# Performance work log

Hardware: AMD Instinct MI355X
Metric: run time of the kernel (lower is better)

Reference implementation:

```python
import jax, jax.numpy as jnp
import numpy as np


def setup_inputs() -> dict:
    key = jax.random.key(0)
    k1, k2, k3, k4 = jax.random.split(key, 4)
    B, D_vis, E, N = 512, 4096, 1024, 512
    vf = jax.random.normal(k1, (B, D_vis), dtype=jnp.float32)
    p_lfs = jax.random.normal(k2, (B, E), dtype=jnp.float32)
    n_lfs = jax.random.normal(k3, (N, E), dtype=jnp.float32)
    W = jax.random.normal(k4, (E, D_vis), dtype=jnp.float32) * (1.0 / np.sqrt(D_vis))
    b = jnp.zeros((E,), dtype=jnp.float32)
    return {"vf": vf, "p_lfs": p_lfs, "n_lfs": n_lfs, "W": W, "b": b}


def _partial_order_sim(hypers, hypos):
    # -||relu(hypers - hypos)||_2 along last dim
    act = jax.nn.relu(hypers - hypos)
    return -jnp.sqrt(jnp.sum(act * act, axis=-1))


def reference(vf, p_lfs, n_lfs, W, b):
    # vf: [B, D_vis], W: [E, D_vis] -> vf_emb: [B, E]
    vf_emb = jnp.einsum("bd,ed->be", vf, W) + b
    # positive scores: [B]
    p_scores = _partial_order_sim(p_lfs, vf_emb)
    # negative scores, batched over B: n_lfs [N,E] vs vf_emb [B,E] -> [B,N]
    n_scores = _partial_order_sim(n_lfs[None, :, :], vf_emb[:, None, :])
    # score_stack: [B, 1+N]
    return jnp.concatenate([p_scores[:, None], n_scores], axis=1)
```

## Files before the change

kernel.cpp:

```cpp
#include <hip/hip_runtime.h>
#include <hip/hip_bf16.h>

constexpr int B = 512;
constexpr int D = 4096;
constexpr int E = 1024;
constexpr int N = 512;
constexpr int KS = 4;
constexpr int KC = D / KS;
constexpr int NSTEP = KC / 32;
constexpr int ES = 8;
constexpr int EC = E / ES;

typedef __attribute__((ext_vector_type(8))) short bf16x8;
typedef __attribute__((ext_vector_type(4))) float f32x4;
typedef float v2f __attribute__((ext_vector_type(2)));

typedef __attribute__((address_space(3))) void lds_void;
typedef const __attribute__((address_space(1))) void gbl_void;

__device__ __forceinline__ unsigned short f2bf(float f) {
    __hip_bfloat16 h = __float2bfloat16(f);
    return *reinterpret_cast<unsigned short*>(&h);
}

__global__ __launch_bounds__(256) void cvt_all(
    const float* __restrict__ vf, const float* __restrict__ W,
    unsigned short* __restrict__ vfB, unsigned short* __restrict__ WB)
{
    const int bid = blockIdx.x;
    const float* src;
    unsigned short* dst;
    int i;
    if (bid < 1024) { src = vf; dst = vfB; i = (bid * 256 + threadIdx.x) * 8; }
    else           { src = W;  dst = WB;  i = ((bid - 1024) * 256 + threadIdx.x) * 8; }
    float4 v0 = *(const float4*)(src + i);
    float4 v1 = *(const float4*)(src + i + 4);
    bf16x8 o;
    o[0] = (short)f2bf(v0.x); o[1] = (short)f2bf(v0.y);
    o[2] = (short)f2bf(v0.z); o[3] = (short)f2bf(v0.w);
    o[4] = (short)f2bf(v1.x); o[5] = (short)f2bf(v1.y);
    o[6] = (short)f2bf(v1.z); o[7] = (short)f2bf(v1.w);
    *(bf16x8*)(dst + i) = o;
}

__global__ __launch_bounds__(64) void gemm_lds(
    const unsigned short* __restrict__ vf,
    const unsigned short* __restrict__ W,
    float* __restrict__ part)
{
    __shared__ unsigned short sA[2][2048];
    __shared__ unsigned short sB[2][2048];

    const int L  = threadIdx.x;
    const int n0 = blockIdx.x * 64;
    const int m0 = blockIdx.y * 64;
    const int ks = blockIdx.z;

    const int subrow = L >> 2;
    const int qstg = (L & 3) ^ ((L >> 2) & 3) ^ ((L >> 4) & 3);
    const int kbeg = ks * KC;
    const unsigned short* aSrc[4];
    const unsigned short* bSrc[4];
    #pragma unroll
    for (int c = 0; c < 4; ++c) {
        aSrc[c] = vf + (size_t)(m0 + c * 16 + subrow) * D + kbeg + qstg * 8;
        bSrc[c] = W  + (size_t)(n0 + c * 16 + subrow) * D + kbeg + qstg * 8;
    }

    const int r16 = L & 15;
    const int quad = L >> 4;
    const int swz = quad ^ (r16 & 3) ^ ((r16 >> 2) & 3);
    const int aoff = r16 * 64 + swz * 16;

    f32x4 acc[4][4] = {};

    auto issue = [&](int step, int buf) {
        const size_t koff = (size_t)step * 32;
        #pragma unroll
        for (int c = 0; c < 4; ++c) {
            __builtin_amdgcn_global_load_lds(
                (gbl_void*)(aSrc[c] + koff),
                (lds_void*)((char*)&sA[buf][0] + c * 1024), 16, 0, 0);
            __builtin_amdgcn_global_load_lds(
                (gbl_void*)(bSrc[c] + koff),
                (lds_void*)((char*)&sB[buf][0] + c * 1024), 16, 0, 0);
        }
    };

    issue(0, 0);
    issue(1, 1);

    #pragma unroll 1
    for (int s = 0; s < NSTEP; ++s) {
        const int buf = s & 1;
        if (s == NSTEP - 1) __builtin_amdgcn_s_waitcnt(0x0F70);
        else                __builtin_amdgcn_s_waitcnt(0x0F78);

        bf16x8 af[4], bf_[4];
        #pragma unroll
        for (int i = 0; i < 4; ++i)
            af[i] = *(const bf16x8*)((const char*)&sA[buf][0] + i * 1024 + aoff);
        #pragma unroll
        for (int j = 0; j < 4; ++j)
            bf_[j] = *(const bf16x8*)((const char*)&sB[buf][0] + j * 1024 + aoff);

        #pragma unroll
        for (int i = 0; i < 4; ++i)
            #pragma unroll
            for (int j = 0; j < 4; ++j)
                acc[i][j] = __builtin_amdgcn_mfma_f32_16x16x32_bf16(
                    af[i], bf_[j], acc[i][j], 0, 0, 0);

        if (s + 2 < NSTEP) issue(s + 2, buf);
    }

    float* po = part + (size_t)ks * B * E;
    #pragma unroll
    for (int j = 0; j < 4; ++j) {
        const int col = n0 + j * 16 + r16;
        #pragma unroll
        for (int i = 0; i < 4; ++i) {
            const int row = m0 + i * 16 + quad * 4;
            #pragma unroll
            for (int r = 0; r < 4; ++r)
                po[(size_t)(row + r) * E + col] = acc[i][j][r];
        }
    }
}

__global__ __launch_bounds__(256) void reduce_emb(
    const float* __restrict__ part, const float* __restrict__ bias,
    float* __restrict__ emb)
{
    const int idx = (blockIdx.x * 256 + threadIdx.x) * 4;
    const int col = idx & (E - 1);
    float4 s = *(const float4*)(bias + col);
    #pragma unroll
    for (int ks = 0; ks < KS; ++ks) {
        float4 p = *(const float4*)(part + (size_t)ks * B * E + idx);
        s.x += p.x; s.y += p.y; s.z += p.z; s.w += p.w;
    }
    *(float4*)(emb + idx) = s;
}

__global__ __launch_bounds__(256, 2) void scores_part(
    const float* __restrict__ emb,
    const float* __restrict__ n_lfs,
    float* __restrict__ pn)
{
    constexpr int LDW = EC + 2;
    __shared__ float eS[64 * LDW];
    __shared__ float nS[64 * LDW];

    const int t  = threadIdx.x;
    const int n0 = blockIdx.x * 64;
    const int b0 = blockIdx.y * 64;
    const int e0 = blockIdx.z * EC;

    {
        const int row = t >> 2;
        const int cb  = (t & 3) * 32;
        const float* ep = emb   + (size_t)(b0 + row) * E + e0 + cb;
        const float* np = n_lfs + (size_t)(n0 + row) * E + e0 + cb;
        float* ed = &eS[row * LDW + cb];
        float* nd = &nS[row * LDW + cb];
        #pragma unroll
        for (int q = 0; q < 8; ++q) {
            float4 v = *(const float4*)(ep + q * 4);
            float4 w = *(const float4*)(np + q * 4);
            *(v2f*)(ed + q * 4)     = (v2f){v.x, v.y};
            *(v2f*)(ed + q * 4 + 2) = (v2f){v.z, v.w};
            *(v2f*)(nd + q * 4)     = (v2f){w.x, w.y};
            *(v2f*)(nd + q * 4 + 2) = (v2f){w.z, w.w};
        }
    }
    __syncthreads();

    const int ty = t >> 4;
    const int tx = t & 15;

    const v2f z = {0.f, 0.f};
    v2f acc[4][4] = {{z,z,z,z},{z,z,z,z},{z,z,z,z},{z,z,z,z}};

    #pragma unroll 4
    for (int e = 0; e < EC; e += 2) {
        v2f a[4], c[4];
        #pragma unroll
        for (int r = 0; r < 4; ++r)
            a[r] = *(const v2f*)&eS[(ty + 16 * r) * LDW + e];
        #pragma unroll
        for (int q = 0; q < 4; ++q)
            c[q] = *(const v2f*)&nS[(tx + 16 * q) * LDW + e];
        #pragma unroll
        for (int r = 0; r < 4; ++r)
            #pragma unroll
            for (int q = 0; q < 4; ++q) {
                v2f d = c[q] - a[r];
                d = __builtin_elementwise_max(d, z);
                acc[r][q] = __builtin_elementwise_fma(d, d, acc[r][q]);
            }
    }

    float* po = pn + (size_t)blockIdx.z * B * N;
    #pragma unroll
    for (int r = 0; r < 4; ++r) {
        const size_t ob = (size_t)(b0 + ty + 16 * r) * N;
        #pragma unroll
        for (int q = 0; q < 4; ++q)
            po[ob + n0 + tx + 16 * q] = acc[r][q].x + acc[r][q].y;
    }
}

__global__ __launch_bounds__(256) void scores_final(
    const float* __restrict__ pn,
    const float* __restrict__ emb,
    const float* __restrict__ p_lfs,
    float* __restrict__ out)
{
    const int t = threadIdx.x;
    if (blockIdx.x < 1024) {
        const int i = blockIdx.x * 256 + t;
        const int b = i >> 9;
        const int n = i & (N - 1);
        float s = 0.f;
        #pragma unroll
        for (int z = 0; z < ES; ++z)
            s += pn[(size_t)z * B * N + i];
        out[(size_t)b * 513 + 1 + n] = -sqrtf(s);
        return;
    }
    const int b0 = (blockIdx.x - 1024) * 32;
    const int r = t >> 3;
    const int g = t & 7;
    const float* pr = p_lfs + (size_t)(b0 + r) * E;
    const float* er = emb   + (size_t)(b0 + r) * E;
    float acc = 0.f;
    for (int e = g * 4; e < E; e += 32) {
        float4 p = *(const float4*)(pr + e);
        float4 v = *(const float4*)(er + e);
        float d;
        d = p.x - v.x; d = fmaxf(d, 0.f); acc = fmaf(d, d, acc);
        d = p.y - v.y; d = fmaxf(d, 0.f); acc = fmaf(d, d, acc);
        d = p.z - v.z; d = fmaxf(d, 0.f); acc = fmaf(d, d, acc);
        d = p.w - v.w; d = fmaxf(d, 0.f); acc = fmaf(d, d, acc);
    }
    #pragma unroll
    for (int off = 4; off; off >>= 1) acc += __shfl_down(acc, off, 8);
    if (g == 0) out[(size_t)(b0 + r) * 513] = -sqrtf(acc);
}

extern "C" void kernel_launch(void* const* d_in, const int* in_sizes, int n_in,
                              void* d_out, int out_size, void* d_ws, size_t ws_size,
                              hipStream_t stream) {
    const float* vf    = (const float*)d_in[0];
    const float* p_lfs = (const float*)d_in[1];
    const float* n_lfs = (const float*)d_in[2];
    const float* W     = (const float*)d_in[3];
    const float* bias  = (const float*)d_in[4];
    float* out = (float*)d_out;

    char* ws = (char*)d_ws;
    float*          pg  = (float*)ws;
    float*          pn  = (float*)ws;
    unsigned short* vfB = (unsigned short*)(ws + ((size_t)8 << 20));
    unsigned short* WB  = (unsigned short*)(ws + ((size_t)12 << 20));
    float*          emb = (float*)(ws + ((size_t)20 << 20));

    cvt_all<<<3072, 256, 0, stream>>>(vf, W, vfB, WB);

    dim3 g1(E / 64, B / 64, KS);
    gemm_lds<<<g1, 64, 0, stream>>>(vfB, WB, pg);

    reduce_emb<<<(B * E) / 1024, 256, 0, stream>>>(pg, bias, emb);

    dim3 g3(N / 64, B / 64, ES);
    scores_part<<<g3, 256, 0, stream>>>(emb, n_lfs, pn);

    scores_final<<<1024 + B / 32, 256, 0, stream>>>(pn, emb, p_lfs, out);
}
```

Measured before the change: 137.2 us.

## Fuse pipeline into one persistent cooperative kernel with grid syncs

Replaces the five-kernel launch sequence with a single cooperative kernel of 256 blocks that runs conversion, split-K GEMM, reduction, partial scores and the final reduction as phases separated by grid.sync. The work split changes as well: the GEMM now uses 8 K-splits with 64x32 per-wave tiles, and the score phase loops over 4 E-chunks per block, giving 4 partial planes. This removes launch gaps and tail effects between kernels, but it caps parallelism at 256 blocks and adds grid-wide barrier costs. The old multi-kernel path is kept as a fallback if the cooperative launch fails.

```diff
diff --git a/kernel.cpp b/kernel.cpp
--- a/kernel.cpp
+++ b/kernel.cpp
@@ -1,15 +1,13 @@
 #include <hip/hip_runtime.h>
 #include <hip/hip_bf16.h>
+#include <hip/hip_cooperative_groups.h>
+
+namespace cg = cooperative_groups;
 
 constexpr int B = 512;
 constexpr int D = 4096;
 constexpr int E = 1024;
 constexpr int N = 512;
-constexpr int KS = 4;
-constexpr int KC = D / KS;
-constexpr int NSTEP = KC / 32;
-constexpr int ES = 8;
-constexpr int EC = E / ES;
 
 typedef __attribute__((ext_vector_type(8))) short bf16x8;
 typedef __attribute__((ext_vector_type(4))) float f32x4;
@@ -22,6 +20,271 @@
     __hip_bfloat16 h = __float2bfloat16(f);
     return *reinterpret_cast<unsigned short*>(&h);
 }
+
+constexpr int KS = 8;
+constexpr int KC = D / KS;
+constexpr int NSTEP = KC / 32;
+constexpr int EC = 64;
+constexpr int LDW = EC + 2;
+constexpr int NPLANE = 4;
+
+__global__ __launch_bounds__(256, 2) void mega(
+    const float* __restrict__ vf,
+    const float* __restrict__ p_lfs,
+    const float* __restrict__ n_lfs,
+    const float* __restrict__ W,
+    const float* __restrict__ bias,
+    float* __restrict__ out,
+    char* __restrict__ ws)
+{
+    float*          pg  = (float*)ws;
+    float*          pn  = (float*)ws;
+    unsigned short* vfB = (unsigned short*)(ws + ((size_t)16 << 20));
+    unsigned short* WB  = (unsigned short*)(ws + ((size_t)20 << 20));
+    float*          emb = (float*)(ws + ((size_t)28 << 20));
+
+    __shared__ __align__(16) char smem[49152];
+
+    const int t   = threadIdx.x;
+    const int bid = blockIdx.x;
+    const int g   = bid * 256 + t;
+    cg::grid_group grid = cg::this_grid();
+
+    #pragma unroll
+    for (int k = 0; k < 12; ++k) {
+        const int c = g + k * 65536;
+        const float* src;
+        unsigned short* dst;
+        int i;
+        if (c < 262144) { src = vf; dst = vfB; i = c * 8; }
+        else            { src = W;  dst = WB;  i = (c - 262144) * 8; }
+        float4 v0 = *(const float4*)(src + i);
+        float4 v1 = *(const float4*)(src + i + 4);
+        bf16x8 o;
+        o[0] = (short)f2bf(v0.x); o[1] = (short)f2bf(v0.y);
+        o[2] = (short)f2bf(v0.z); o[3] = (short)f2bf(v0.w);
+        o[4] = (short)f2bf(v1.x); o[5] = (short)f2bf(v1.y);
+        o[6] = (short)f2bf(v1.z); o[7] = (short)f2bf(v1.w);
+        *(bf16x8*)(dst + i) = o;
+    }
+
+    grid.sync();
+
+    {
+        const int w = t >> 6;
+        const int L = t & 63;
+        char* base = smem + w * 12288;
+
+        const int subrow = L >> 2;
+        const int qstg = (L & 3) ^ ((L >> 2) & 3) ^ ((L >> 4) & 3);
+        const int r16 = L & 15;
+        const int quad = L >> 4;
+        const int swz = quad ^ (r16 & 3) ^ ((r16 >> 2) & 3);
+        const int aoff = r16 * 64 + swz * 16;
+
+        #pragma unroll 1
+        for (int pass = 0; pass < 2; ++pass) {
+            const int task = (bid * 4 + w) + pass * 1024;
+            const int n0 = (task & 31) * 32;
+            const int m0 = ((task >> 5) & 7) * 64;
+            const int ks = task >> 8;
+            const int kbeg = ks * KC;
+
+            const unsigned short* aSrc[4];
+            const unsigned short* bSrc[2];
+            #pragma unroll
+            for (int c = 0; c < 4; ++c)
+                aSrc[c] = vfB + (size_t)(m0 + c * 16 + subrow) * D + kbeg + qstg * 8;
+            #pragma unroll
+            for (int c = 0; c < 2; ++c)
+                bSrc[c] = WB  + (size_t)(n0 + c * 16 + subrow) * D + kbeg + qstg * 8;
+
+            auto issue = [&](int step, int buf) {
+                const size_t koff = (size_t)step * 32;
+                #pragma unroll
+                for (int c = 0; c < 4; ++c)
+                    __builtin_amdgcn_global_load_lds(
+                        (gbl_void*)(aSrc[c] + koff),
+                        (lds_void*)(base + buf * 4096 + c * 1024), 16, 0, 0);
+                #pragma unroll
+                for (int c = 0; c < 2; ++c)
+                    __builtin_amdgcn_global_load_lds(
+                        (gbl_void*)(bSrc[c] + koff),
+                        (lds_void*)(base + 8192 + buf * 2048 + c * 1024), 16, 0, 0);
+            };
+
+            f32x4 acc[4][2] = {};
+
+            issue(0, 0);
+            issue(1, 1);
+
+            #pragma unroll 1
+            for (int s = 0; s < NSTEP; ++s) {
+                const int buf = s & 1;
+                if (s == NSTEP - 1) __builtin_amdgcn_s_waitcnt(0x0F70);
+                else                __builtin_amdgcn_s_waitcnt(0x0F76);
+
+                bf16x8 af[4], bfr[2];
+                #pragma unroll
+                for (int i = 0; i < 4; ++i)
+                    af[i] = *(const bf16x8*)(base + buf * 4096 + i * 1024 + aoff);
+                #pragma unroll
+                for (int j = 0; j < 2; ++j)
+                    bfr[j] = *(const bf16x8*)(base + 8192 + buf * 2048 + j * 1024 + aoff);
+
+                #pragma unroll
+                for (int i = 0; i < 4; ++i)
+                    #pragma unroll
+                    for (int j = 0; j < 2; ++j)
+                        acc[i][j] = __builtin_amdgcn_mfma_f32_16x16x32_bf16(
+                            af[i], bfr[j], acc[i][j], 0, 0, 0);
+
+                if (s + 2 < NSTEP) issue(s + 2, buf);
+            }
+
+            float* po = pg + (size_t)ks * B * E;
+            #pragma unroll
+            for (int j = 0; j < 2; ++j) {
+                const int col = n0 + j * 16 + r16;
+                #pragma unroll
+                for (int i = 0; i < 4; ++i) {
+                    const int row = m0 + i * 16 + quad * 4;
+                    #pragma unroll
+                    for (int r = 0; r < 4; ++r)
+                        po[(size_t)(row + r) * E + col] = acc[i][j][r];
+                }
+            }
+        }
+    }
+
+    grid.sync();
+
+    #pragma unroll
+    for (int k = 0; k < 2; ++k) {
+        const int idx = (g + k * 65536) * 4;
+        const int col = idx & (E - 1);
+        float4 s = *(const float4*)(bias + col);
+        #pragma unroll
+        for (int z = 0; z < KS; ++z) {
+            float4 p = *(const float4*)(pg + (size_t)z * B * E + idx);
+            s.x += p.x; s.y += p.y; s.z += p.z; s.w += p.w;
+        }
+        *(float4*)(emb + idx) = s;
+    }
+
+    grid.sync();
+
+    {
+        float* eS = (float*)smem;
+        float* nS = eS + 64 * LDW;
+
+        const int n0 = (bid & 7) * 64;
+        const int b0 = ((bid >> 3) & 7) * 64;
+        const int c0 = bid >> 6;
+
+        const int row = t >> 2;
+        const int cb  = (t & 3) * 16;
+        const int ty = t >> 4;
+        const int tx = t & 15;
+
+        const v2f z = {0.f, 0.f};
+        v2f acc[4][4] = {{z,z,z,z},{z,z,z,z},{z,z,z,z},{z,z,z,z}};
+
+        #pragma unroll 1
+        for (int p = 0; p < 4; ++p) {
+            const int e0 = (c0 + 4 * p) * EC;
+            __syncthreads();
+            {
+                const float* ep = emb   + (size_t)(b0 + row) * E + e0 + cb;
+                const float* np = n_lfs + (size_t)(n0 + row) * E + e0 + cb;
+                float* ed = &eS[row * LDW + cb];
+                float* nd = &nS[row * LDW + cb];
+                #pragma unroll
+                for (int q = 0; q < 4; ++q) {
+                    float4 v  = *(const float4*)(ep + q * 4);
+                    float4 wv = *(const float4*)(np + q * 4);
+                    *(v2f*)(ed + q * 4)     = (v2f){v.x, v.y};
+                    *(v2f*)(ed + q * 4 + 2) = (v2f){v.z, v.w};
+                    *(v2f*)(nd + q * 4)     = (v2f){wv.x, wv.y};
+                    *(v2f*)(nd + q * 4 + 2) = (v2f){wv.z, wv.w};
+                }
+            }
+            __syncthreads();
+
+            #pragma unroll 4
+            for (int e = 0; e < EC; e += 2) {
+                v2f a[4], c[4];
+                #pragma unroll
+                for (int r = 0; r < 4; ++r)
+                    a[r] = *(const v2f*)&eS[(ty + 16 * r) * LDW + e];
+                #pragma unroll
+                for (int q = 0; q < 4; ++q)
+                    c[q] = *(const v2f*)&nS[(tx + 16 * q) * LDW + e];
+                #pragma unroll
+                for (int r = 0; r < 4; ++r)
+                    #pragma unroll
+                    for (int q = 0; q < 4; ++q) {
+                        v2f d = c[q] - a[r];
+                        d = __builtin_elementwise_max(d, z);
+                        acc[r][q] = __builtin_elementwise_fma(d, d, acc[r][q]);
+                    }
+            }
+        }
+
+        float* po = pn + (size_t)c0 * B * N;
+        #pragma unroll
+        for (int r = 0; r < 4; ++r) {
+            const size_t ob = (size_t)(b0 + ty + 16 * r) * N;
+            #pragma unroll
+            for (int q = 0; q < 4; ++q)
+                po[ob + n0 + tx + 16 * q] = acc[r][q].x + acc[r][q].y;
+        }
+    }
+
+    grid.sync();
+
+    {
+        const int i = g * 4;
+        const int b = i >> 9;
+        const int n = i & (N - 1);
+        float4 s = {0.f, 0.f, 0.f, 0.f};
+        #pragma unroll
+        for (int z = 0; z < NPLANE; ++z) {
+            float4 p = *(const float4*)(pn + (size_t)z * B * N + i);
+            s.x += p.x; s.y += p.y; s.z += p.z; s.w += p.w;
+        }
+        float* o = out + (size_t)b * 513 + 1 + n;
+        o[0] = -sqrtf(s.x); o[1] = -sqrtf(s.y);
+        o[2] = -sqrtf(s.z); o[3] = -sqrtf(s.w);
+
+        if (bid < 16) {
+            const int b0 = bid * 32;
+            const int r = t >> 3;
+            const int gq = t & 7;
+            const float* pr = p_lfs + (size_t)(b0 + r) * E;
+            const float* er = emb   + (size_t)(b0 + r) * E;
+            float acc = 0.f;
+            for (int e = gq * 4; e < E; e += 32) {
+                float4 p = *(const float4*)(pr + e);
+                float4 v = *(const float4*)(er + e);
+                float d;
+                d = p.x - v.x; d = fmaxf(d, 0.f); acc = fmaf(d, d, acc);
+                d = p.y - v.y; d = fmaxf(d, 0.f); acc = fmaf(d, d, acc);
+                d = p.z - v.z; d = fmaxf(d, 0.f); acc = fmaf(d, d, acc);
+                d = p.w - v.w; d = fmaxf(d, 0.f); acc = fmaf(d, d, acc);
+            }
+            #pragma unroll
+            for (int off = 4; off; off >>= 1) acc += __shfl_down(acc, off, 8);
+            if (gq == 0) out[(size_t)(b0 + r) * 513] = -sqrtf(acc);
+        }
+    }
+}
+
+constexpr int FKS = 4;
+constexpr int FKC = D / FKS;
+constexpr int FNS = FKC / 32;
+constexpr int FES = 8;
+constexpr int FEC = E / FES;
 
 __global__ __launch_bounds__(256) void cvt_all(
     const float* __restrict__ vf, const float* __restrict__ W,
@@ -58,7 +321,7 @@
 
     const int subrow = L >> 2;
     const int qstg = (L & 3) ^ ((L >> 2) & 3) ^ ((L >> 4) & 3);
-    const int kbeg = ks * KC;
+    const int kbeg = ks * FKC;
     const unsigned short* aSrc[4];
     const unsigned short* bSrc[4];
     #pragma unroll
@@ -91,10 +354,10 @@
     issue(1, 1);
 
     #pragma unroll 1
-    for (int s = 0; s < NSTEP; ++s) {
+    for (int s = 0; s < FNS; ++s) {
         const int buf = s & 1;
-        if (s == NSTEP - 1) __builtin_amdgcn_s_waitcnt(0x0F70);
-        else                __builtin_amdgcn_s_waitcnt(0x0F78);
+        if (s == FNS - 1) __builtin_amdgcn_s_waitcnt(0x0F70);
+        else              __builtin_amdgcn_s_waitcnt(0x0F78);
 
         bf16x8 af[4], bf_[4];
         #pragma unroll
@@ -111,7 +374,7 @@
                 acc[i][j] = __builtin_amdgcn_mfma_f32_16x16x32_bf16(
                     af[i], bf_[j], acc[i][j], 0, 0, 0);
 
-        if (s + 2 < NSTEP) issue(s + 2, buf);
+        if (s + 2 < FNS) issue(s + 2, buf);
     }
 
     float* po = part + (size_t)ks * B * E;
@@ -136,7 +399,7 @@
     const int col = idx & (E - 1);
     float4 s = *(const float4*)(bias + col);
     #pragma unroll
-    for (int ks = 0; ks < KS; ++ks) {
+    for (int ks = 0; ks < FKS; ++ks) {
         float4 p = *(const float4*)(part + (size_t)ks * B * E + idx);
         s.x += p.x; s.y += p.y; s.z += p.z; s.w += p.w;
     }
@@ -148,22 +411,22 @@
     const float* __restrict__ n_lfs,
     float* __restrict__ pn)
 {
-    constexpr int LDW = EC + 2;
-    __shared__ float eS[64 * LDW];
-    __shared__ float nS[64 * LDW];
+    constexpr int W2 = FEC + 2;
+    __shared__ float eS[64 * W2];
+    __shared__ float nS[64 * W2];
 
     const int t  = threadIdx.x;
     const int n0 = blockIdx.x * 64;
     const int b0 = blockIdx.y * 64;
-    const int e0 = blockIdx.z * EC;
+    const int e0 = blockIdx.z * FEC;
 
     {
         const int row = t >> 2;
         const int cb  = (t & 3) * 32;
         const float* ep = emb   + (size_t)(b0 + row) * E + e0 + cb;
         const float* np = n_lfs + (size_t)(n0 + row) * E + e0 + cb;
-        float* ed = &eS[row * LDW + cb];
-        float* nd = &nS[row * LDW + cb];
+        float* ed = &eS[row * W2 + cb];
+        float* nd = &nS[row * W2 + cb];
         #pragma unroll
         for (int q = 0; q < 8; ++q) {
             float4 v = *(const float4*)(ep + q * 4);
@@ -183,14 +446,14 @@
     v2f acc[4][4] = {{z,z,z,z},{z,z,z,z},{z,z,z,z},{z,z,z,z}};
 
     #pragma unroll 4
-    for (int e = 0; e < EC; e += 2) {
+    for (int e = 0; e < FEC; e += 2) {
         v2f a[4], c[4];
         #pragma unroll
         for (int r = 0; r < 4; ++r)
-            a[r] = *(const v2f*)&eS[(ty + 16 * r) * LDW + e];
+            a[r] = *(const v2f*)&eS[(ty + 16 * r) * W2 + e];
         #pragma unroll
         for (int q = 0; q < 4; ++q)
-            c[q] = *(const v2f*)&nS[(tx + 16 * q) * LDW + e];
+            c[q] = *(const v2f*)&nS[(tx + 16 * q) * W2 + e];
         #pragma unroll
         for (int r = 0; r < 4; ++r)
             #pragma unroll
@@ -224,7 +487,7 @@
         const int n = i & (N - 1);
         float s = 0.f;
         #pragma unroll
-        for (int z = 0; z < ES; ++z)
+        for (int z = 0; z < FES; ++z)
             s += pn[(size_t)z * B * N + i];
         out[(size_t)b * 513 + 1 + n] = -sqrtf(s);
         return;
@@ -258,8 +521,15 @@
     const float* W     = (const float*)d_in[3];
     const float* bias  = (const float*)d_in[4];
     float* out = (float*)d_out;
-
-    char* ws = (char*)d_ws;
+    char* ws   = (char*)d_ws;
+
+    void* args[] = {(void*)&vf, (void*)&p_lfs, (void*)&n_lfs, (void*)&W,
+                    (void*)&bias, (void*)&out, (void*)&ws};
+    hipError_t err = hipLaunchCooperativeKernel((const void*)mega, dim3(256),
+                                                dim3(256), args, 0, stream);
+    if (err == hipSuccess) return;
+    (void)hipGetLastError();
+
     float*          pg  = (float*)ws;
     float*          pn  = (float*)ws;
     unsigned short* vfB = (unsigned short*)(ws + ((size_t)8 << 20));
@@ -267,14 +537,10 @@
     float*          emb = (float*)(ws + ((size_t)20 << 20));
 
     cvt_all<<<3072, 256, 0, stream>>>(vf, W, vfB, WB);
-
-    dim3 g1(E / 64, B / 64, KS);
+    dim3 g1(E / 64, B / 64, FKS);
     gemm_lds<<<g1, 64, 0, stream>>>(vfB, WB, pg);
-
     reduce_emb<<<(B * E) / 1024, 256, 0, stream>>>(pg, bias, emb);
-
-    dim3 g3(N / 64, B / 64, ES);
+    dim3 g3(N / 64, B / 64, FES);
     scores_part<<<g3, 256, 0, stream>>>(emb, n_lfs, pn);
-
     scores_final<<<1024 + B / 32, 256, 0, stream>>>(pn, emb, p_lfs, out);
 }
```

After: 284.9 us. 108% more time.

## Fuse split-K reduction, score computation and final reduction into one kernel

Applied to the files above, without the earlier changes.

Removes the reduce_emb and scores_final kernels. The score kernel now sums the split-K GEMM partials plus bias while staging the embedding into shared memory. An extra column of blocks computes the positive scores. The final reduction over E-slices is done by the last-arriving block per tile, using atomic tickets and threadfences. This saves two launches and the global round trip of the embedding, but it reads the GEMM partials redundantly (once per n-tile) and adds an atomic counter memset.

```diff
diff --git a/kernel.cpp b/kernel.cpp
--- a/kernel.cpp
+++ b/kernel.cpp
@@ -10,6 +10,7 @@
 constexpr int NSTEP = KC / 32;
 constexpr int ES = 8;
 constexpr int EC = E / ES;
+constexpr int LDW = EC + 2;
 
 typedef __attribute__((ext_vector_type(8))) short bf16x8;
 typedef __attribute__((ext_vector_type(4))) float f32x4;
@@ -128,50 +129,90 @@
     }
 }
 
-__global__ __launch_bounds__(256) void reduce_emb(
-    const float* __restrict__ part, const float* __restrict__ bias,
-    float* __restrict__ emb)
+__global__ __launch_bounds__(256, 2) void scores_fused(
+    const float* __restrict__ pg,
+    const float* __restrict__ bias,
+    const float* __restrict__ n_lfs,
+    const float* __restrict__ p_lfs,
+    float* __restrict__ pn,
+    float* __restrict__ pp,
+    int* __restrict__ tk,
+    float* __restrict__ out)
 {
-    const int idx = (blockIdx.x * 256 + threadIdx.x) * 4;
-    const int col = idx & (E - 1);
-    float4 s = *(const float4*)(bias + col);
-    #pragma unroll
-    for (int ks = 0; ks < KS; ++ks) {
-        float4 p = *(const float4*)(part + (size_t)ks * B * E + idx);
-        s.x += p.x; s.y += p.y; s.z += p.z; s.w += p.w;
-    }
-    *(float4*)(emb + idx) = s;
-}
-
-__global__ __launch_bounds__(256, 2) void scores_part(
-    const float* __restrict__ emb,
-    const float* __restrict__ n_lfs,
-    float* __restrict__ pn)
-{
-    constexpr int LDW = EC + 2;
     __shared__ float eS[64 * LDW];
     __shared__ float nS[64 * LDW];
-
-    const int t  = threadIdx.x;
+    __shared__ int lastFlag;
+
+    const int t   = threadIdx.x;
+    const int b0i = blockIdx.y;
+    const int z   = blockIdx.z;
+    const int b0  = b0i * 64;
+    const int e0  = z * EC;
+
+    if (blockIdx.x == 8) {
+        const int row = t >> 2;
+        const int sub = t & 3;
+        const int b   = b0 + row;
+        const int eb  = e0 + sub * 32;
+        float acc = 0.f;
+        #pragma unroll
+        for (int q = 0; q < 8; ++q) {
+            const int e = eb + q * 4;
+            float4 s = *(const float4*)(bias + e);
+            #pragma unroll
+            for (int ks = 0; ks < KS; ++ks) {
+                float4 p = *(const float4*)(pg + (size_t)ks * B * E + (size_t)b * E + e);
+                s.x += p.x; s.y += p.y; s.z += p.z; s.w += p.w;
+            }
+            float4 p = *(const float4*)(p_lfs + (size_t)b * E + e);
+            float d;
+            d = p.x - s.x; d = fmaxf(d, 0.f); acc = fmaf(d, d, acc);
+            d = p.y - s.y; d = fmaxf(d, 0.f); acc = fmaf(d, d, acc);
+            d = p.z - s.z; d = fmaxf(d, 0.f); acc = fmaf(d, d, acc);
+            d = p.w - s.w; d = fmaxf(d, 0.f); acc = fmaf(d, d, acc);
+        }
+        acc += __shfl_down(acc, 2, 4);
+        acc += __shfl_down(acc, 1, 4);
+        if (sub == 0) pp[z * B + b] = acc;
+
+        __syncthreads();
+        __threadfence();
+        if (t == 0) lastFlag = (atomicAdd(&tk[64 + b0i], 1) == ES - 1);
+        __syncthreads();
+        if (lastFlag) {
+            __threadfence();
+            if (t < 64) {
+                const int b2 = b0 + t;
+                float s = 0.f;
+                #pragma unroll
+                for (int zz = 0; zz < ES; ++zz) s += pp[zz * B + b2];
+                out[(size_t)b2 * 513] = -sqrtf(s);
+            }
+        }
+        return;
+    }
+
     const int n0 = blockIdx.x * 64;
-    const int b0 = blockIdx.y * 64;
-    const int e0 = blockIdx.z * EC;
-
     {
         const int row = t >> 2;
         const int cb  = (t & 3) * 32;
-        const float* ep = emb   + (size_t)(b0 + row) * E + e0 + cb;
         const float* np = n_lfs + (size_t)(n0 + row) * E + e0 + cb;
+        const size_t ebase = (size_t)(b0 + row) * E + e0 + cb;
         float* ed = &eS[row * LDW + cb];
         float* nd = &nS[row * LDW + cb];
         #pragma unroll
         for (int q = 0; q < 8; ++q) {
-            float4 v = *(const float4*)(ep + q * 4);
-            float4 w = *(const float4*)(np + q * 4);
+            float4 v = *(const float4*)(bias + ((ebase + q * 4) & (E - 1)));
+            #pragma unroll
+            for (int ks = 0; ks < KS; ++ks) {
+                float4 p = *(const float4*)(pg + (size_t)ks * B * E + ebase + q * 4);
+                v.x += p.x; v.y += p.y; v.z += p.z; v.w += p.w;
+            }
+            float4 wv = *(const float4*)(np + q * 4);
             *(v2f*)(ed + q * 4)     = (v2f){v.x, v.y};
             *(v2f*)(ed + q * 4 + 2) = (v2f){v.z, v.w};
-            *(v2f*)(nd + q * 4)     = (v2f){w.x, w.y};
-            *(v2f*)(nd + q * 4 + 2) = (v2f){w.z, w.w};
+            *(v2f*)(nd + q * 4)     = (v2f){wv.x, wv.y};
+            *(v2f*)(nd + q * 4 + 2) = (v2f){wv.z, wv.w};
         }
     }
     __syncthreads();
@@ -179,8 +220,8 @@
     const int ty = t >> 4;
     const int tx = t & 15;
 
-    const v2f z = {0.f, 0.f};
-    v2f acc[4][4] = {{z,z,z,z},{z,z,z,z},{z,z,z,z},{z,z,z,z}};
+    const v2f zv = {0.f, 0.f};
+    v2f acc[4][4] = {{zv,zv,zv,zv},{zv,zv,zv,zv},{zv,zv,zv,zv},{zv,zv,zv,zv}};
 
     #pragma unroll 4
     for (int e = 0; e < EC; e += 2) {
@@ -196,12 +237,12 @@
             #pragma unroll
             for (int q = 0; q < 4; ++q) {
                 v2f d = c[q] - a[r];
-                d = __builtin_elementwise_max(d, z);
+                d = __builtin_elementwise_max(d, zv);
                 acc[r][q] = __builtin_elementwise_fma(d, d, acc[r][q]);
             }
     }
 
-    float* po = pn + (size_t)blockIdx.z * B * N;
+    float* po = pn + (size_t)z * B * N;
     #pragma unroll
     for (int r = 0; r < 4; ++r) {
         const size_t ob = (size_t)(b0 + ty + 16 * r) * N;
@@ -209,44 +250,27 @@
         for (int q = 0; q < 4; ++q)
             po[ob + n0 + tx + 16 * q] = acc[r][q].x + acc[r][q].y;
     }
-}
-
-__global__ __launch_bounds__(256) void scores_final(
-    const float* __restrict__ pn,
-    const float* __restrict__ emb,
-    const float* __restrict__ p_lfs,
-    float* __restrict__ out)
-{
-    const int t = threadIdx.x;
-    if (blockIdx.x < 1024) {
-        const int i = blockIdx.x * 256 + t;
-        const int b = i >> 9;
-        const int n = i & (N - 1);
-        float s = 0.f;
-        #pragma unroll
-        for (int z = 0; z < ES; ++z)
-            s += pn[(size_t)z * B * N + i];
-        out[(size_t)b * 513 + 1 + n] = -sqrtf(s);
-        return;
-    }
-    const int b0 = (blockIdx.x - 1024) * 32;
-    const int r = t >> 3;
-    const int g = t & 7;
-    const float* pr = p_lfs + (size_t)(b0 + r) * E;
-    const float* er = emb   + (size_t)(b0 + r) * E;
-    float acc = 0.f;
-    for (int e = g * 4; e < E; e += 32) {
-        float4 p = *(const float4*)(pr + e);
-        float4 v = *(const float4*)(er + e);
-        float d;
-        d = p.x - v.x; d = fmaxf(d, 0.f); acc = fmaf(d, d, acc);
-        d = p.y - v.y; d = fmaxf(d, 0.f); acc = fmaf(d, d, acc);
-        d = p.z - v.z; d = fmaxf(d, 0.f); acc = fmaf(d, d, acc);
-        d = p.w - v.w; d = fmaxf(d, 0.f); acc = fmaf(d, d, acc);
-    }
-    #pragma unroll
-    for (int off = 4; off; off >>= 1) acc += __shfl_down(acc, off, 8);
-    if (g == 0) out[(size_t)(b0 + r) * 513] = -sqrtf(acc);
+
+    __syncthreads();
+    __threadfence();
+    if (t == 0) lastFlag = (atomicAdd(&tk[b0i * 8 + blockIdx.x], 1) == ES - 1);
+    __syncthreads();
+    if (lastFlag) {
+        __threadfence();
+        #pragma unroll
+        for (int r = 0; r < 4; ++r) {
+            const int b = b0 + ty + 16 * r;
+            #pragma unroll
+            for (int q = 0; q < 4; ++q) {
+                const int n = n0 + tx + 16 * q;
+                float s = 0.f;
+                #pragma unroll
+                for (int zz = 0; zz < ES; ++zz)
+                    s += pn[(size_t)zz * B * N + (size_t)b * N + n];
+                out[(size_t)b * 513 + 1 + n] = -sqrtf(s);
+            }
+        }
+    }
 }
 
 extern "C" void kernel_launch(void* const* d_in, const int* in_sizes, int n_in,
@@ -261,20 +285,19 @@
 
     char* ws = (char*)d_ws;
     float*          pg  = (float*)ws;
-    float*          pn  = (float*)ws;
-    unsigned short* vfB = (unsigned short*)(ws + ((size_t)8 << 20));
-    unsigned short* WB  = (unsigned short*)(ws + ((size_t)12 << 20));
-    float*          emb = (float*)(ws + ((size_t)20 << 20));
+    float*          pn  = (float*)(ws + ((size_t)8 << 20));
+    float*          pp  = (float*)(ws + ((size_t)16 << 20));
+    int*            tk  = (int*)  (ws + ((size_t)17 << 20));
+    unsigned short* vfB = (unsigned short*)(ws + ((size_t)18 << 20));
+    unsigned short* WB  = (unsigned short*)(ws + ((size_t)22 << 20));
+
+    hipMemsetAsync(tk, 0, 72 * sizeof(int), stream);
 
     cvt_all<<<3072, 256, 0, stream>>>(vf, W, vfB, WB);
 
     dim3 g1(E / 64, B / 64, KS);
     gemm_lds<<<g1, 64, 0, stream>>>(vfB, WB, pg);
 
-    reduce_emb<<<(B * E) / 1024, 256, 0, stream>>>(pg, bias, emb);
-
-    dim3 g3(N / 64, B / 64, ES);
-    scores_part<<<g3, 256, 0, stream>>>(emb, n_lfs, pn);
-
-    scores_final<<<1024 + B / 32, 256, 0, stream>>>(pn, emb, p_lfs, out);
-}
+    dim3 g2(9, B / 64, ES);
+    scores_fused<<<g2, 256, 0, stream>>>(pg, bias, n_lfs, p_lfs, pn, pp, tk, out);
+}
```

Measured after the change: 219.5 us. +60.0%, slower.

## Drop split-K GEMM, fuse bias reduction, deepen LDS pipeline to four stages

Applied to the files above, without the earlier changes.

Removes the split-K partitioning so each block computes the full K range and writes the final embedding with bias added directly. This eliminates the reduce kernel and the partial-sum round trip through memory. The main loop uses a four-buffer LDS ring with register-level double buffering of fragments to overlap loads and MFMAs. The trade-off is a 4x smaller grid (128 single-wave blocks), which reduces parallelism across CUs and lengthens each block's serial K loop.

```diff
diff --git a/kernel.cpp b/kernel.cpp
--- a/kernel.cpp
+++ b/kernel.cpp
@@ -5,11 +5,9 @@
 constexpr int D = 4096;
 constexpr int E = 1024;
 constexpr int N = 512;
-constexpr int KS = 4;
-constexpr int KC = D / KS;
-constexpr int NSTEP = KC / 32;
 constexpr int ES = 8;
 constexpr int EC = E / ES;
+constexpr int LDW = EC + 2;
 
 typedef __attribute__((ext_vector_type(8))) short bf16x8;
 typedef __attribute__((ext_vector_type(4))) float f32x4;
@@ -43,28 +41,27 @@
     *(bf16x8*)(dst + i) = o;
 }
 
-__global__ __launch_bounds__(64) void gemm_lds(
+__global__ __launch_bounds__(64) void gemm_direct(
     const unsigned short* __restrict__ vf,
     const unsigned short* __restrict__ W,
-    float* __restrict__ part)
-{
-    __shared__ unsigned short sA[2][2048];
-    __shared__ unsigned short sB[2][2048];
+    const float* __restrict__ bias,
+    float* __restrict__ emb)
+{
+    __shared__ unsigned short sA[4][2048];
+    __shared__ unsigned short sB[4][2048];
 
     const int L  = threadIdx.x;
     const int n0 = blockIdx.x * 64;
     const int m0 = blockIdx.y * 64;
-    const int ks = blockIdx.z;
 
     const int subrow = L >> 2;
     const int qstg = (L & 3) ^ ((L >> 2) & 3) ^ ((L >> 4) & 3);
-    const int kbeg = ks * KC;
     const unsigned short* aSrc[4];
     const unsigned short* bSrc[4];
     #pragma unroll
     for (int c = 0; c < 4; ++c) {
-        aSrc[c] = vf + (size_t)(m0 + c * 16 + subrow) * D + kbeg + qstg * 8;
-        bSrc[c] = W  + (size_t)(n0 + c * 16 + subrow) * D + kbeg + qstg * 8;
+        aSrc[c] = vf + (size_t)(m0 + c * 16 + subrow) * D + qstg * 8;
+        bSrc[c] = W  + (size_t)(n0 + c * 16 + subrow) * D + qstg * 8;
     }
 
     const int r16 = L & 15;
@@ -74,7 +71,8 @@
 
     f32x4 acc[4][4] = {};
 
-    auto issue = [&](int step, int buf) {
+    auto issue = [&](int step) {
+        const int buf = step & 3;
         const size_t koff = (size_t)step * 32;
         #pragma unroll
         for (int c = 0; c < 4; ++c) {
@@ -87,60 +85,65 @@
         }
     };
 
-    issue(0, 0);
-    issue(1, 1);
-
-    #pragma unroll 1
-    for (int s = 0; s < NSTEP; ++s) {
-        const int buf = s & 1;
-        if (s == NSTEP - 1) __builtin_amdgcn_s_waitcnt(0x0F70);
-        else                __builtin_amdgcn_s_waitcnt(0x0F78);
-
-        bf16x8 af[4], bf_[4];
+    bf16x8 a0[4], b0[4], a1[4], b1[4];
+
+    auto readFrags = [&](int step, bf16x8* af, bf16x8* bf_) {
+        const int buf = step & 3;
         #pragma unroll
         for (int i = 0; i < 4; ++i)
             af[i] = *(const bf16x8*)((const char*)&sA[buf][0] + i * 1024 + aoff);
         #pragma unroll
         for (int j = 0; j < 4; ++j)
             bf_[j] = *(const bf16x8*)((const char*)&sB[buf][0] + j * 1024 + aoff);
-
+    };
+
+    auto mfma16 = [&](bf16x8* af, bf16x8* bf_) {
         #pragma unroll
         for (int i = 0; i < 4; ++i)
             #pragma unroll
             for (int j = 0; j < 4; ++j)
                 acc[i][j] = __builtin_amdgcn_mfma_f32_16x16x32_bf16(
                     af[i], bf_[j], acc[i][j], 0, 0, 0);
-
-        if (s + 2 < NSTEP) issue(s + 2, buf);
-    }
-
-    float* po = part + (size_t)ks * B * E;
+    };
+
+    issue(0); issue(1); issue(2); issue(3);
+    __builtin_amdgcn_s_waitcnt(0x4F78);
+    readFrags(0, a0, b0);
+
+    #pragma unroll 1
+    for (int s = 0; s < 124; s += 2) {
+        __builtin_amdgcn_s_waitcnt(0x4F70);
+        readFrags(s + 1, a1, b1);
+        mfma16(a0, b0);
+        issue(s + 4);
+        __builtin_amdgcn_s_waitcnt(0x4F70);
+        readFrags(s + 2, a0, b0);
+        mfma16(a1, b1);
+        issue(s + 5);
+    }
+    __builtin_amdgcn_s_waitcnt(0x4F70);
+    readFrags(125, a1, b1);
+    mfma16(a0, b0);
+    __builtin_amdgcn_s_waitcnt(0x0F78);
+    readFrags(126, a0, b0);
+    mfma16(a1, b1);
+    __builtin_amdgcn_s_waitcnt(0x0F70);
+    readFrags(127, a1, b1);
+    mfma16(a0, b0);
+    mfma16(a1, b1);
+
     #pragma unroll
     for (int j = 0; j < 4; ++j) {
         const int col = n0 + j * 16 + r16;
+        const float bv = bias[col];
         #pragma unroll
         for (int i = 0; i < 4; ++i) {
             const int row = m0 + i * 16 + quad * 4;
             #pragma unroll
             for (int r = 0; r < 4; ++r)
-                po[(size_t)(row + r) * E + col] = acc[i][j][r];
+                emb[(size_t)(row + r) * E + col] = acc[i][j][r] + bv;
         }
     }
-}
-
-__global__ __launch_bounds__(256) void reduce_emb(
-    const float* __restrict__ part, const float* __restrict__ bias,
-    float* __restrict__ emb)
-{
-    const int idx = (blockIdx.x * 256 + threadIdx.x) * 4;
-    const int col = idx & (E - 1);
-    float4 s = *(const float4*)(bias + col);
-    #pragma unroll
-    for (int ks = 0; ks < KS; ++ks) {
-        float4 p = *(const float4*)(part + (size_t)ks * B * E + idx);
-        s.x += p.x; s.y += p.y; s.z += p.z; s.w += p.w;
-    }
-    *(float4*)(emb + idx) = s;
 }
 
 __global__ __launch_bounds__(256, 2) void scores_part(
@@ -148,7 +151,6 @@
     const float* __restrict__ n_lfs,
     float* __restrict__ pn)
 {
-    constexpr int LDW = EC + 2;
     __shared__ float eS[64 * LDW];
     __shared__ float nS[64 * LDW];
 
@@ -260,7 +262,6 @@
     float* out = (float*)d_out;
 
     char* ws = (char*)d_ws;
-    float*          pg  = (float*)ws;
     float*          pn  = (float*)ws;
     unsigned short* vfB = (unsigned short*)(ws + ((size_t)8 << 20));
     unsigned short* WB  = (unsigned short*)(ws + ((size_t)12 << 20));
@@ -268,10 +269,8 @@
 
     cvt_all<<<3072, 256, 0, stream>>>(vf, W, vfB, WB);
 
-    dim3 g1(E / 64, B / 64, KS);
-    gemm_lds<<<g1, 64, 0, stream>>>(vfB, WB, pg);
-
-    reduce_emb<<<(B * E) / 1024, 256, 0, stream>>>(pg, bias, emb);
+    dim3 g1(E / 64, B / 64);
+    gemm_direct<<<g1, 64, 0, stream>>>(vfB, WB, bias, emb);
 
     dim3 g3(N / 64, B / 64, ES);
     scores_part<<<g3, 256, 0, stream>>>(emb, n_lfs, pn);
```

Result: slower. 161.8 us (+17.9%).
